# Kernel optimization log

Measured on AMD Instinct MI355X. Metric: run time of the kernel, lower is better.

## Reference

```python
import jax, jax.numpy as jnp
import numpy as np
import math

D_MODEL = 640
HEAD_DIM = 64
N_HEADS = 14
N_KV_HEADS = 2
HPK = N_HEADS // N_KV_HEADS  # 7
EPS = 1e-5
T = 2048
D_HALF = HEAD_DIM // 2


def setup_inputs() -> dict:
    key = jax.random.key(0)
    ks = jax.random.split(key, 10)
    x = jax.random.normal(ks[0], (1, D_MODEL, 1, T), dtype=jnp.float32)
    # rope tables: realistic cos/sin from standard rotary frequencies
    inv_freq = 1.0 / (10000.0 ** (jnp.arange(0, HEAD_DIM, 2, dtype=jnp.float32) / HEAD_DIM))
    ang = jnp.arange(T, dtype=jnp.float32)[:, None] * inv_freq[None, :]  # (T, 32)
    rope_cos = jnp.cos(ang)
    rope_sin = jnp.sin(ang)
    # causal additive mask (T, T)
    causal = jnp.tril(jnp.ones((T, T), dtype=bool))
    attn_mask = jnp.where(causal, 0.0, -1e9).astype(jnp.float32)
    norm_w = 1.0 + 0.02 * jax.random.normal(ks[1], (D_MODEL,), dtype=jnp.float32)
    qkv_dim = (N_HEADS + 2 * N_KV_HEADS) * HEAD_DIM  # 1152
    qkv_w = jax.random.normal(ks[2], (qkv_dim, D_MODEL), dtype=jnp.float32) * (D_MODEL ** -0.5)
    qkv_b = 0.02 * jax.random.normal(ks[3], (qkv_dim,), dtype=jnp.float32)
    o_w = jax.random.normal(ks[4], (D_MODEL, N_HEADS * HEAD_DIM), dtype=jnp.float32) * ((N_HEADS * HEAD_DIM) ** -0.5)
    o_b = 0.02 * jax.random.normal(ks[5], (D_MODEL,), dtype=jnp.float32)
    sinks = jax.random.normal(ks[6], (N_HEADS,), dtype=jnp.float32)
    return {"x": x, "rope_cos": rope_cos, "rope_sin": rope_sin, "attn_mask": attn_mask,
            "norm_w": norm_w, "qkv_w": qkv_w, "qkv_b": qkv_b, "o_w": o_w, "o_b": o_b,
            "sinks": sinks}


def _apply_rope(xf, n_heads, rope_cos, rope_sin):
    # xf: (1, T, n_heads*dh) -> interleaved rotary
    xr = xf.reshape(1, T, n_heads, HEAD_DIM)
    x1 = xr[..., 0::2]  # (1, T, n, d_half)
    x2 = xr[..., 1::2]
    cos = rope_cos[None, :, None, :]
    sin = rope_sin[None, :, None, :]
    o1 = x1 * cos - x2 * sin
    o2 = x2 * cos + x1 * sin
    return jnp.stack((o1, o2), axis=-1).reshape(1, T, n_heads * HEAD_DIM)


def reference(x, rope_cos, rope_sin, attn_mask, norm_w, qkv_w, qkv_b, o_w, o_b, sinks):
    nh, nkv, hpk, dh = N_HEADS, N_KV_HEADS, HPK, HEAD_DIM
    residual = x
    # RMSNorm over channel dim (axis=1)
    var = jnp.mean(x * x, axis=1, keepdims=True)
    normed = x * jax.lax.rsqrt(var + EPS) * norm_w.reshape(1, -1, 1, 1)
    # fused 1x1 conv QKV: (1, D, T) -> (1, T, qkv_dim)
    n2 = normed[:, :, 0, :]  # (1, D, T)
    qkv = jnp.einsum('bct,oc->bto', n2, qkv_w) + qkv_b
    q_dim = nh * dh
    kv_dim = nkv * dh
    q = qkv[:, :, :q_dim]
    k = qkv[:, :, q_dim:q_dim + kv_dim]
    v = qkv[:, :, q_dim + kv_dim:]
    q = _apply_rope(q, nh, rope_cos, rope_sin)
    k = _apply_rope(k, nkv, rope_cos, rope_sin)
    qk_scale = 1.0 / math.sqrt(math.sqrt(dh))
    q = q * qk_scale
    k = k * qk_scale
    q = q.reshape(1, T, nkv, hpk, dh)
    k = k.reshape(1, T, nkv, dh)
    v = v.reshape(1, T, nkv, dh)
    # GQA scores: (1, nkv, hpk, T, T)
    scores = jnp.einsum('btkgd,bskd->bkgts', q, k)
    scores = scores + attn_mask[None, None, None, :, :]
    # attention-sink logit column appended before softmax
    sink = (sinks * math.log(2.0)).reshape(1, nkv, hpk, 1, 1)
    sink_col = jnp.broadcast_to(sink, (1, nkv, hpk, T, 1))
    scores_with_sink = jnp.concatenate([scores, sink_col], axis=-1)
    attn_w = jax.nn.softmax(scores_with_sink, axis=-1)[..., :-1]
    # weighted values: (1, T, nkv, hpk, dh) -> (1, T, nh*dh)
    attn_out = jnp.einsum('bkgts,bskd->btkgd', attn_w, v).reshape(1, T, nh * dh)
    # output 1x1 conv + residual
    proj = jnp.einsum('bto,do->bdt', attn_out, o_w) + o_b.reshape(1, -1, 1)
    return residual + proj[:, :, None, :]
```

## Files before the change

### kernel.cpp

```cpp
#include <hip/hip_runtime.h>
#include <math.h>

#define T 2048
#define DM 640
#define NH 14
#define NKV 2
#define HPK 7
#define HD 64
#define QDIM 896
#define QKV_DIM 1152

constexpr float QK_SCALE2 = 0.35355339059327373f * 1.2011224087864498f;
constexpr float EPSF = 1e-5f;

typedef __attribute__((ext_vector_type(8))) short short8;
typedef __attribute__((ext_vector_type(4))) float float4v;
typedef unsigned short ush;

static __device__ __forceinline__ ush f2bf(float f) {
    union { float f; unsigned u; } v; v.f = f;
    unsigned r = v.u + 0x7fffu + ((v.u >> 16) & 1u);
    return (ush)(r >> 16);
}
static __device__ __forceinline__ float bf2f(ush s) {
    union { unsigned u; float f; } v; v.u = ((unsigned)s) << 16;
    return v.f;
}

__global__ __launch_bounds__(256) void rstd_kernel(
    const float* __restrict__ x, float* __restrict__ rstd)
{
    const int t0 = blockIdx.x * 64;
    const int tl = threadIdx.x & 63, cg = threadIdx.x >> 6;
    __shared__ float red[4][64];
    float ss = 0.f;
    for (int c = cg; c < DM; c += 4) {
        const float v = x[(size_t)c * T + t0 + tl];
        ss = fmaf(v, v, ss);
    }
    red[cg][tl] = ss;
    __syncthreads();
    if (threadIdx.x < 64) {
        const float s = red[0][tl] + red[1][tl] + red[2][tl] + red[3][tl];
        rstd[t0 + tl] = rsqrtf(s * (1.0f / DM) + EPSF);
    }
}

__global__ __launch_bounds__(256) void cast2_kernel(
    const float* __restrict__ a, ush* __restrict__ ah, ush* __restrict__ al, int na4,
    const float* __restrict__ b, ush* __restrict__ bh, ush* __restrict__ bl)
{
    const int i = blockIdx.x * 256 + threadIdx.x;
    const float* src; ush *dh, *dl; int j;
    if (i < na4) { src = a; dh = ah; dl = al; j = i; }
    else         { src = b; dh = bh; dl = bl; j = i - na4; }
    const float4 v = ((const float4*)src)[j];
    ushort4 h, l;
    h.x = f2bf(v.x); l.x = f2bf(v.x - bf2f(h.x));
    h.y = f2bf(v.y); l.y = f2bf(v.y - bf2f(h.y));
    h.z = f2bf(v.z); l.z = f2bf(v.z - bf2f(h.z));
    h.w = f2bf(v.w); l.w = f2bf(v.w - bf2f(h.w));
    ((ushort4*)dh)[j] = h;
    ((ushort4*)dl)[j] = l;
}

__global__ __launch_bounds__(256) void xnorm_kernel(
    const float* __restrict__ x, const float* __restrict__ norm_w,
    const float* __restrict__ rstd,
    ush* __restrict__ XnH, ush* __restrict__ XnL)
{
    const int tid = threadIdx.x;
    const int t0 = blockIdx.x * 64;
    const int c0 = blockIdx.y * 64;
    __shared__ float xs[64][65];

    #pragma unroll
    for (int it = 0; it < 4; ++it) {
        const int r = (tid >> 4) + it * 16;
        const int cl = (tid & 15) * 4;
        const float4 v = *(const float4*)&x[(size_t)(c0 + r) * T + t0 + cl];
        xs[r][cl + 0] = v.x; xs[r][cl + 1] = v.y;
        xs[r][cl + 2] = v.z; xs[r][cl + 3] = v.w;
    }
    __syncthreads();
    #pragma unroll
    for (int it = 0; it < 4; ++it) {
        const int tr = (tid >> 4) + it * 16;
        const int cl = (tid & 15) * 4;
        const float rs = rstd[t0 + tr];
        ushort4 h, l;
        const float v0 = xs[cl + 0][tr] * norm_w[c0 + cl + 0] * rs;
        const float v1 = xs[cl + 1][tr] * norm_w[c0 + cl + 1] * rs;
        const float v2 = xs[cl + 2][tr] * norm_w[c0 + cl + 2] * rs;
        const float v3 = xs[cl + 3][tr] * norm_w[c0 + cl + 3] * rs;
        h.x = f2bf(v0); l.x = f2bf(v0 - bf2f(h.x));
        h.y = f2bf(v1); l.y = f2bf(v1 - bf2f(h.y));
        h.z = f2bf(v2); l.z = f2bf(v2 - bf2f(h.z));
        h.w = f2bf(v3); l.w = f2bf(v3 - bf2f(h.w));
        *(ushort4*)&XnH[(size_t)(t0 + tr) * DM + c0 + cl] = h;
        *(ushort4*)&XnL[(size_t)(t0 + tr) * DM + c0 + cl] = l;
    }
}

#define QSX_H 0
#define QSX_L 8192
#define QSW_H 16384
#define QSW_L 24576

__global__ __launch_bounds__(256) void qkv_mfma_kernel(
    const ush* __restrict__ XnH, const ush* __restrict__ XnL,
    const ush* __restrict__ WH, const ush* __restrict__ WL,
    const float* __restrict__ qkv_b, const float* __restrict__ rope_cos,
    const float* __restrict__ rope_sin,
    ush* __restrict__ Qh, ush* __restrict__ Ql,
    ush* __restrict__ Kh, ush* __restrict__ Kl,
    ush* __restrict__ Vth, ush* __restrict__ Vtl)
{
    const int t0 = blockIdx.x * 64;
    const int o0 = blockIdx.y * 64;
    const int tid = threadIdx.x;
    const int wave = tid >> 6, lane = tid & 63;
    const int lg = lane >> 4, lq = lane & 15;
    const int wr = wave >> 1, wc = wave & 1;

    __shared__ __align__(16) unsigned char sm[65536];

    const int srow0 = tid >> 3, srow1 = srow0 + 32, scc = tid & 7;
    const int dst0 = srow0 * 128 + ((scc * 16) ^ ((srow0 & 7) << 4));
    const int dst1 = srow1 * 128 + ((scc * 16) ^ ((srow1 & 7) << 4));

    uint4 xh0, xl0, wh0, wl0, xh1, xl1, wh1, wl1;

#define QLOAD(c_) do { \
    xh0 = *(const uint4*)&XnH[(size_t)(t0 + srow0) * DM + (c_) + scc * 8]; \
    xl0 = *(const uint4*)&XnL[(size_t)(t0 + srow0) * DM + (c_) + scc * 8]; \
    wh0 = *(const uint4*)&WH [(size_t)(o0 + srow0) * DM + (c_) + scc * 8]; \
    wl0 = *(const uint4*)&WL [(size_t)(o0 + srow0) * DM + (c_) + scc * 8]; \
    xh1 = *(const uint4*)&XnH[(size_t)(t0 + srow1) * DM + (c_) + scc * 8]; \
    xl1 = *(const uint4*)&XnL[(size_t)(t0 + srow1) * DM + (c_) + scc * 8]; \
    wh1 = *(const uint4*)&WH [(size_t)(o0 + srow1) * DM + (c_) + scc * 8]; \
    wl1 = *(const uint4*)&WL [(size_t)(o0 + srow1) * DM + (c_) + scc * 8]; \
} while (0)

#define QSTORE(b_) do { \
    *(uint4*)((b_) + QSX_H + dst0) = xh0; \
    *(uint4*)((b_) + QSX_L + dst0) = xl0; \
    *(uint4*)((b_) + QSW_H + dst0) = wh0; \
    *(uint4*)((b_) + QSW_L + dst0) = wl0; \
    *(uint4*)((b_) + QSX_H + dst1) = xh1; \
    *(uint4*)((b_) + QSX_L + dst1) = xl1; \
    *(uint4*)((b_) + QSW_H + dst1) = wh1; \
    *(uint4*)((b_) + QSW_L + dst1) = wl1; \
} while (0)

    float4v acc[2][2];
    acc[0][0] = (float4v)0.f; acc[0][1] = (float4v)0.f;
    acc[1][0] = (float4v)0.f; acc[1][1] = (float4v)0.f;

    QLOAD(0);
    QSTORE(sm);
    int cur = 0;
    for (int s = 0; s < 10; ++s) {
        if (s < 9) QLOAD((s + 1) * 64);
        __syncthreads();
        const unsigned char* smb = sm + cur * 32768;
        #pragma unroll
        for (int kk = 0; kk < 2; ++kk) {
            short8 ah[2], al[2], bh[2], bl[2];
            #pragma unroll
            for (int nt = 0; nt < 2; ++nt) {
                const int row = wc * 32 + nt * 16 + lq;
                const int col = (kk * 64 + lg * 16) ^ ((row & 7) << 4);
                bh[nt] = *(const short8*)(smb + QSX_H + row * 128 + col);
                bl[nt] = *(const short8*)(smb + QSX_L + row * 128 + col);
            }
            #pragma unroll
            for (int mt = 0; mt < 2; ++mt) {
                const int row = wr * 32 + mt * 16 + lq;
                const int col = (kk * 64 + lg * 16) ^ ((row & 7) << 4);
                ah[mt] = *(const short8*)(smb + QSW_H + row * 128 + col);
                al[mt] = *(const short8*)(smb + QSW_L + row * 128 + col);
            }
            #pragma unroll
            for (int mt = 0; mt < 2; ++mt) {
                #pragma unroll
                for (int nt = 0; nt < 2; ++nt) {
                    acc[mt][nt] = __builtin_amdgcn_mfma_f32_16x16x32_bf16(ah[mt], bh[nt], acc[mt][nt], 0, 0, 0);
                    acc[mt][nt] = __builtin_amdgcn_mfma_f32_16x16x32_bf16(ah[mt], bl[nt], acc[mt][nt], 0, 0, 0);
                    acc[mt][nt] = __builtin_amdgcn_mfma_f32_16x16x32_bf16(al[mt], bh[nt], acc[mt][nt], 0, 0, 0);
                }
            }
        }
        if (s < 9) { QSTORE(sm + ((cur ^ 1) * 32768)); cur ^= 1; }
    }
#undef QLOAD
#undef QSTORE

    const int by = blockIdx.y;
    #pragma unroll
    for (int mt = 0; mt < 2; ++mt) {
        const int d0 = wr * 32 + mt * 16 + lg * 4;
        #pragma unroll
        for (int nt = 0; nt < 2; ++nt) {
            const int t = t0 + wc * 32 + nt * 16 + lq;
            if (by < 16) {
                const float e0 = acc[mt][nt][0] + qkv_b[o0 + d0 + 0];
                const float d1 = acc[mt][nt][1] + qkv_b[o0 + d0 + 1];
                const float e2 = acc[mt][nt][2] + qkv_b[o0 + d0 + 2];
                const float d3 = acc[mt][nt][3] + qkv_b[o0 + d0 + 3];
                const float c0v = rope_cos[t * 32 + (d0 >> 1)];
                const float s0v = rope_sin[t * 32 + (d0 >> 1)];
                const float c1v = rope_cos[t * 32 + (d0 >> 1) + 1];
                const float s1v = rope_sin[t * 32 + (d0 >> 1) + 1];
                const float r0 = (e0 * c0v - d1 * s0v) * QK_SCALE2;
                const float r1 = (d1 * c0v + e0 * s0v) * QK_SCALE2;
                const float r2 = (e2 * c1v - d3 * s1v) * QK_SCALE2;
                const float r3 = (d3 * c1v + e2 * s1v) * QK_SCALE2;
                ushort4 h, l;
                h.x = f2bf(r0); l.x = f2bf(r0 - bf2f(h.x));
                h.y = f2bf(r1); l.y = f2bf(r1 - bf2f(h.y));
                h.z = f2bf(r2); l.z = f2bf(r2 - bf2f(h.z));
                h.w = f2bf(r3); l.w = f2bf(r3 - bf2f(h.w));
                if (by < 14) {
                    *(ushort4*)&Qh[((size_t)(by * T + t)) * HD + d0] = h;
                    *(ushort4*)&Ql[((size_t)(by * T + t)) * HD + d0] = l;
                } else {
                    const int h2 = by - 14;
                    *(ushort4*)&Kh[((size_t)(h2 * T + t)) * HD + d0] = h;
                    *(ushort4*)&Kl[((size_t)(h2 * T + t)) * HD + d0] = l;
                }
            } else {
                const int h2 = by - 16;
                #pragma unroll
                for (int j = 0; j < 4; ++j) {
                    const float val = acc[mt][nt][j] + qkv_b[o0 + d0 + j];
                    const ush hh = f2bf(val);
                    Vth[((size_t)(h2 * HD + d0 + j)) * T + t] = hh;
                    Vtl[((size_t)(h2 * HD + d0 + j)) * T + t] = f2bf(val - bf2f(hh));
                }
            }
        }
    }
}

__global__ __launch_bounds__(256) void attn_mfma_kernel(
    const ush* __restrict__ Qh, const ush* __restrict__ Ql,
    const ush* __restrict__ Kh, const ush* __restrict__ Kl,
    const ush* __restrict__ Vth, const ush* __restrict__ Vtl,
    const float* __restrict__ sinks,
    ush* __restrict__ AOH, ush* __restrict__ AOL)
{
    const int qt = 31 - (int)blockIdx.x;
    const int h  = blockIdx.y;
    const int kvh = h / HPK;
    const int tid = threadIdx.x;
    const int wave = tid >> 6, lane = tid & 63;
    const int lg = lane >> 4, lq = lane & 15;
    const int qbase = qt * 64 + wave * 16;
    const int myq = qbase + lq;

    __shared__ __align__(16) unsigned char sm[2 * 32768 + 4 * 2304];
    unsigned int* Pl = (unsigned int*)(sm + 65536) + wave * (16 * 36);

    short8 qf[2][2];
    #pragma unroll
    for (int kk = 0; kk < 2; ++kk) {
        const size_t qoff = ((size_t)(h * T + myq)) * HD + kk * 32 + lg * 8;
        qf[kk][0] = *(const short8*)&Qh[qoff];
        qf[kk][1] = *(const short8*)&Ql[qoff];
    }

    float4v oacc[4];
    #pragma unroll
    for (int dt = 0; dt < 4; ++dt) oacc[dt] = (float4v)0.f;

    float m2 = sinks[h];
    float l  = 1.0f;

    const ush* Khp = Kh + (size_t)kvh * T * HD;
    const ush* Klp = Kl + (size_t)kvh * T * HD;
    const ush* Vhp = Vth + (size_t)kvh * HD * T;
    const ush* Vlp = Vtl + (size_t)kvh * HD * T;

    const int srow0 = tid >> 3, srow1 = srow0 + 32, scc = tid & 7;
    const int dst0 = srow0 * 128 + ((scc * 16) ^ ((srow0 & 7) << 4));
    const int dst1 = srow1 * 128 + ((scc * 16) ^ ((srow1 & 7) << 4));

    uint4 rk0h, rk0l, rv0h, rv0l, rk1h, rk1l, rv1h, rv1l;

#define ALOAD(kb_) do { \
    rk0h = *(const uint4*)(Khp + (size_t)((kb_) + srow0) * HD + scc * 8); \
    rk0l = *(const uint4*)(Klp + (size_t)((kb_) + srow0) * HD + scc * 8); \
    rv0h = *(const uint4*)(Vhp + (size_t)srow0 * T + (kb_) + scc * 8); \
    rv0l = *(const uint4*)(Vlp + (size_t)srow0 * T + (kb_) + scc * 8); \
    rk1h = *(const uint4*)(Khp + (size_t)((kb_) + srow1) * HD + scc * 8); \
    rk1l = *(const uint4*)(Klp + (size_t)((kb_) + srow1) * HD + scc * 8); \
    rv1h = *(const uint4*)(Vhp + (size_t)srow1 * T + (kb_) + scc * 8); \
    rv1l = *(const uint4*)(Vlp + (size_t)srow1 * T + (kb_) + scc * 8); \
} while (0)

#define ASTORE(b_) do { \
    *(uint4*)((b_) + 0     + dst0) = rk0h; \
    *(uint4*)((b_) + 8192  + dst0) = rk0l; \
    *(uint4*)((b_) + 16384 + dst0) = rv0h; \
    *(uint4*)((b_) + 24576 + dst0) = rv0l; \
    *(uint4*)((b_) + 0     + dst1) = rk1h; \
    *(uint4*)((b_) + 8192  + dst1) = rk1l; \
    *(uint4*)((b_) + 16384 + dst1) = rv1h; \
    *(uint4*)((b_) + 24576 + dst1) = rv1l; \
} while (0)

    ALOAD(0);
    ASTORE(sm);
    int cur = 0;

    for (int kt = 0; kt <= qt; ++kt) {
        const int kb = kt * 64;
        const bool more = (kt < qt);
        if (more) ALOAD(kb + 64);
        __syncthreads();
        unsigned char* smb = sm + cur * 32768;

        float4v st[4];
        #pragma unroll
        for (int t = 0; t < 4; ++t) st[t] = (float4v)0.f;
        #pragma unroll
        for (int t = 0; t < 4; ++t) {
            const int row = t * 16 + lq;
            const int rb = row * 128;
            const int sw = (row & 7) << 4;
            #pragma unroll
            for (int kk = 0; kk < 2; ++kk) {
                const int col = (kk * 64 + lg * 16) ^ sw;
                const short8 ah = *(const short8*)(smb + rb + col);
                const short8 al = *(const short8*)(smb + 8192 + rb + col);
                st[t] = __builtin_amdgcn_mfma_f32_16x16x32_bf16(ah, qf[kk][0], st[t], 0, 0, 0);
                st[t] = __builtin_amdgcn_mfma_f32_16x16x32_bf16(ah, qf[kk][1], st[t], 0, 0, 0);
                st[t] = __builtin_amdgcn_mfma_f32_16x16x32_bf16(al, qf[kk][0], st[t], 0, 0, 0);
            }
        }

        float pmax = -3e38f;
        #pragma unroll
        for (int t = 0; t < 4; ++t) {
            #pragma unroll
            for (int j = 0; j < 4; ++j) {
                const int key = kb + 16 * t + 4 * lg + j;
                const float s = (key > myq) ? -3e38f : st[t][j];
                st[t][j] = s;
                pmax = fmaxf(pmax, s);
            }
        }
        pmax = fmaxf(pmax, __shfl_xor(pmax, 16));
        pmax = fmaxf(pmax, __shfl_xor(pmax, 32));
        if (__any(pmax > m2)) {
            const float mnew = fmaxf(m2, pmax);
            const float corr = exp2f(m2 - mnew);
            l *= corr;
            #pragma unroll
            for (int dt = 0; dt < 4; ++dt) oacc[dt] *= corr;
            m2 = mnew;
        }
        float psum = 0.f;
        #pragma unroll
        for (int t = 0; t < 4; ++t) {
            #pragma unroll
            for (int j = 0; j < 4; ++j) {
                const float p = exp2f(st[t][j] - m2);
                st[t][j] = p;
                psum += p;
            }
        }
        psum += __shfl_xor(psum, 16);
        psum += __shfl_xor(psum, 32);
        l += psum;

        #pragma unroll
        for (int t = 0; t < 4; ++t) {
            #pragma unroll
            for (int j2 = 0; j2 < 2; ++j2) {
                const unsigned int u = (unsigned int)f2bf(st[t][2 * j2]) |
                                       ((unsigned int)f2bf(st[t][2 * j2 + 1]) << 16);
                Pl[lq * 36 + t * 8 + lg * 2 + j2] = u;
            }
        }

        #pragma unroll
        for (int c = 0; c < 2; ++c) {
            const short8 pf = *(const short8*)&Pl[lq * 36 + c * 16 + lg * 4];
            #pragma unroll
            for (int dt = 0; dt < 4; ++dt) {
                const int row = dt * 16 + lq;
                const int rb = row * 128;
                const int col = (c * 64 + lg * 16) ^ ((row & 7) << 4);
                const short8 vh = *(const short8*)(smb + 16384 + rb + col);
                const short8 vl = *(const short8*)(smb + 24576 + rb + col);
                oacc[dt] = __builtin_amdgcn_mfma_f32_16x16x32_bf16(vh, pf, oacc[dt], 0, 0, 0);
                oacc[dt] = __builtin_amdgcn_mfma_f32_16x16x32_bf16(vl, pf, oacc[dt], 0, 0, 0);
            }
        }

        if (more) { ASTORE(sm + ((cur ^ 1) * 32768)); cur ^= 1; }
    }
#undef ALOAD
#undef ASTORE

    const float invl = 1.0f / l;
    const int r = qbase + lq;
    const size_t obase = (size_t)r * QDIM + h * 64;
    #pragma unroll
    for (int dt = 0; dt < 4; ++dt) {
        ushort4 hh, ll;
        #pragma unroll
        for (int j = 0; j < 4; ++j) {
            const float val = oacc[dt][j] * invl;
            const ush hv = f2bf(val);
            ((ush*)&hh)[j] = hv;
            ((ush*)&ll)[j] = f2bf(val - bf2f(hv));
        }
        *(ushort4*)&AOH[obase + dt * 16 + lg * 4] = hh;
        *(ushort4*)&AOL[obase + dt * 16 + lg * 4] = ll;
    }
}

#define PSA_H 0
#define PSA_L 8192
#define PSW_H 16384
#define PSW_L 24576

__global__ __launch_bounds__(256) void oproj_mfma_kernel(
    const ush* __restrict__ AOH, const ush* __restrict__ AOL,
    const ush* __restrict__ OWH, const ush* __restrict__ OWL,
    const float* __restrict__ o_b, const float* __restrict__ x,
    float* __restrict__ out)
{
    const int t0 = blockIdx.x * 64;
    const int c0 = blockIdx.y * 64;
    const int tid = threadIdx.x;
    const int wave = tid >> 6, lane = tid & 63;
    const int lg = lane >> 4, lq = lane & 15;
    const int wr = wave >> 1, wc = wave & 1;

    __shared__ __align__(16) unsigned char sm[65536];

    const int srow0 = tid >> 3, srow1 = srow0 + 32, scc = tid & 7;
    const int dst0 = srow0 * 128 + ((scc * 16) ^ ((srow0 & 7) << 4));
    const int dst1 = srow1 * 128 + ((scc * 16) ^ ((srow1 & 7) << 4));

    uint4 xh0, xl0, wh0, wl0, xh1, xl1, wh1, wl1;

#define PLOAD(k_) do { \
    xh0 = *(const uint4*)&AOH[(size_t)(t0 + srow0) * QDIM + (k_) + scc * 8]; \
    xl0 = *(const uint4*)&AOL[(size_t)(t0 + srow0) * QDIM + (k_) + scc * 8]; \
    wh0 = *(const uint4*)&OWH[(size_t)(c0 + srow0) * QDIM + (k_) + scc * 8]; \
    wl0 = *(const uint4*)&OWL[(size_t)(c0 + srow0) * QDIM + (k_) + scc * 8]; \
    xh1 = *(const uint4*)&AOH[(size_t)(t0 + srow1) * QDIM + (k_) + scc * 8]; \
    xl1 = *(const uint4*)&AOL[(size_t)(t0 + srow1) * QDIM + (k_) + scc * 8]; \
    wh1 = *(const uint4*)&OWH[(size_t)(c0 + srow1) * QDIM + (k_) + scc * 8]; \
    wl1 = *(const uint4*)&OWL[(size_t)(c0 + srow1) * QDIM + (k_) + scc * 8]; \
} while (0)

#define PSTORE(b_) do { \
    *(uint4*)((b_) + PSA_H + dst0) = xh0; \
    *(uint4*)((b_) + PSA_L + dst0) = xl0; \
    *(uint4*)((b_) + PSW_H + dst0) = wh0; \
    *(uint4*)((b_) + PSW_L + dst0) = wl0; \
    *(uint4*)((b_) + PSA_H + dst1) = xh1; \
    *(uint4*)((b_) + PSA_L + dst1) = xl1; \
    *(uint4*)((b_) + PSW_H + dst1) = wh1; \
    *(uint4*)((b_) + PSW_L + dst1) = wl1; \
} while (0)

    float4v acc[2][2];
    acc[0][0] = (float4v)0.f; acc[0][1] = (float4v)0.f;
    acc[1][0] = (float4v)0.f; acc[1][1] = (float4v)0.f;

    PLOAD(0);
    PSTORE(sm);
    int cur = 0;
    for (int s = 0; s < 14; ++s) {
        if (s < 13) PLOAD((s + 1) * 64);
        __syncthreads();
        const unsigned char* smb = sm + cur * 32768;
        #pragma unroll
        for (int kk = 0; kk < 2; ++kk) {
            short8 ah[2], al[2], bh[2], bl[2];
            #pragma unroll
            for (int nt = 0; nt < 2; ++nt) {
                const int row = wc * 32 + nt * 16 + lq;
                const int col = (kk * 64 + lg * 16) ^ ((row & 7) << 4);
                bh[nt] = *(const short8*)(smb + PSA_H + row * 128 + col);
                bl[nt] = *(const short8*)(smb + PSA_L + row * 128 + col);
            }
            #pragma unroll
            for (int mt = 0; mt < 2; ++mt) {
                const int row = wr * 32 + mt * 16 + lq;
                const int col = (kk * 64 + lg * 16) ^ ((row & 7) << 4);
                ah[mt] = *(const short8*)(smb + PSW_H + row * 128 + col);
                al[mt] = *(const short8*)(smb + PSW_L + row * 128 + col);
            }
            #pragma unroll
            for (int mt = 0; mt < 2; ++mt) {
                #pragma unroll
                for (int nt = 0; nt < 2; ++nt) {
                    acc[mt][nt] = __builtin_amdgcn_mfma_f32_16x16x32_bf16(ah[mt], bh[nt], acc[mt][nt], 0, 0, 0);
                    acc[mt][nt] = __builtin_amdgcn_mfma_f32_16x16x32_bf16(ah[mt], bl[nt], acc[mt][nt], 0, 0, 0);
                    acc[mt][nt] = __builtin_amdgcn_mfma_f32_16x16x32_bf16(al[mt], bh[nt], acc[mt][nt], 0, 0, 0);
                }
            }
        }
        if (s < 13) { PSTORE(sm + ((cur ^ 1) * 32768)); cur ^= 1; }
    }
#undef PLOAD
#undef PSTORE

    #pragma unroll
    for (int mt = 0; mt < 2; ++mt) {
        const int cb = c0 + wr * 32 + mt * 16 + lg * 4;
        #pragma unroll
        for (int nt = 0; nt < 2; ++nt) {
            const int t = t0 + wc * 32 + nt * 16 + lq;
            #pragma unroll
            for (int j = 0; j < 4; ++j) {
                const int c = cb + j;
                out[(size_t)c * T + t] = acc[mt][nt][j] + o_b[c] + x[(size_t)c * T + t];
            }
        }
    }
}

extern "C" void kernel_launch(void* const* d_in, const int* in_sizes, int n_in,
                              void* d_out, int out_size, void* d_ws, size_t ws_size,
                              hipStream_t stream) {
    const float* x        = (const float*)d_in[0];
    const float* rope_cos = (const float*)d_in[1];
    const float* rope_sin = (const float*)d_in[2];
    const float* norm_w   = (const float*)d_in[4];
    const float* qkv_w    = (const float*)d_in[5];
    const float* qkv_b    = (const float*)d_in[6];
    const float* o_w      = (const float*)d_in[7];
    const float* o_b      = (const float*)d_in[8];
    const float* sinks    = (const float*)d_in[9];
    float* out = (float*)d_out;

    float* ws   = (float*)d_ws;
    float* rstd = ws;
    ush* bws = (ush*)(rstd + 2048);
    ush* Qh  = bws;
    ush* Ql  = Qh  + 1835008;
    ush* Kh  = Ql  + 1835008;
    ush* Kl  = Kh  + 262144;
    ush* Vth = Kl  + 262144;
    ush* Vtl = Vth + 262144;
    ush* XnH = Vtl + 262144;
    ush* XnL = XnH + 1310720;
    ush* WqH = XnL + 1310720;
    ush* WqL = WqH + 737280;
    ush* OWH = WqL + 737280;
    ush* OWL = OWH + 573440;
    ush* AOH = OWL + 573440;
    ush* AOL = AOH + 1835008;

    rstd_kernel<<<32, 256, 0, stream>>>(x, rstd);
    cast2_kernel<<<1280, 256, 0, stream>>>(qkv_w, WqH, WqL, QKV_DIM * DM / 4,
                                           o_w, OWH, OWL);
    xnorm_kernel<<<dim3(32, 10), 256, 0, stream>>>(x, norm_w, rstd, XnH, XnL);
    qkv_mfma_kernel<<<dim3(32, 18), 256, 0, stream>>>(
        XnH, XnL, WqH, WqL, qkv_b, rope_cos, rope_sin, Qh, Ql, Kh, Kl, Vth, Vtl);
    attn_mfma_kernel<<<dim3(32, NH), 256, 0, stream>>>(
        Qh, Ql, Kh, Kl, Vth, Vtl, sinks, AOH, AOL);
    oproj_mfma_kernel<<<dim3(32, 10), 256, 0, stream>>>(AOH, AOL, OWH, OWL, o_b, x, out);
}
```

Measured before the change: 250.8 us.

## Split attention KV range across two blocks and merge with combine kernel

```diff
diff --git a/kernel.cpp b/kernel.cpp
--- a/kernel.cpp
+++ b/kernel.cpp
@@ -161,8 +161,8 @@
     QSTORE(sm);
     int cur = 0;
     for (int s = 0; s < 10; ++s) {
+        __syncthreads();
         if (s < 9) QLOAD((s + 1) * 64);
-        __syncthreads();
         const unsigned char* smb = sm + cur * 32768;
         #pragma unroll
         for (int kk = 0; kk < 2; ++kk) {
@@ -248,10 +248,11 @@
     const ush* __restrict__ Kh, const ush* __restrict__ Kl,
     const ush* __restrict__ Vth, const ush* __restrict__ Vtl,
     const float* __restrict__ sinks,
-    ush* __restrict__ AOH, ush* __restrict__ AOL)
+    float* __restrict__ Opart, float* __restrict__ Mpart, float* __restrict__ Lpart)
 {
     const int qt = 31 - (int)blockIdx.x;
     const int h  = blockIdx.y;
+    const int kc = blockIdx.z;
     const int kvh = h / HPK;
     const int tid = threadIdx.x;
     const int wave = tid >> 6, lane = tid & 63;
@@ -274,8 +275,9 @@
     #pragma unroll
     for (int dt = 0; dt < 4; ++dt) oacc[dt] = (float4v)0.f;
 
-    float m2 = sinks[h];
-    float l  = 1.0f;
+    float m2, l;
+    if (kc == 0) { m2 = sinks[h]; l = 1.0f; }
+    else         { m2 = -3e38f;   l = 0.0f; }
 
     const ush* Khp = Kh + (size_t)kvh * T * HD;
     const ush* Klp = Kl + (size_t)kvh * T * HD;
@@ -310,15 +312,15 @@
     *(uint4*)((b_) + 24576 + dst1) = rv1l; \
 } while (0)
 
-    ALOAD(0);
-    ASTORE(sm);
+    const int nt_cnt = (qt >= kc) ? ((qt - kc) >> 1) + 1 : 0;
+    if (nt_cnt > 0) { ALOAD(kc * 64); ASTORE(sm); }
     int cur = 0;
 
-    for (int kt = 0; kt <= qt; ++kt) {
+    for (int i = 0; i < nt_cnt; ++i) {
+        const int kt = kc + 2 * i;
         const int kb = kt * 64;
-        const bool more = (kt < qt);
-        if (more) ALOAD(kb + 64);
         __syncthreads();
+        if (i + 1 < nt_cnt) ALOAD(kb + 128);
         unsigned char* smb = sm + cur * 32768;
 
         float4v st[4];
@@ -400,26 +402,58 @@
             }
         }
 
-        if (more) { ASTORE(sm + ((cur ^ 1) * 32768)); cur ^= 1; }
+        if (i + 1 < nt_cnt) { ASTORE(sm + ((cur ^ 1) * 32768)); cur ^= 1; }
     }
 #undef ALOAD
 #undef ASTORE
 
-    const float invl = 1.0f / l;
     const int r = qbase + lq;
-    const size_t obase = (size_t)r * QDIM + h * 64;
+    const int pb = (h * 2 + kc) * 64;
     #pragma unroll
     for (int dt = 0; dt < 4; ++dt) {
+        #pragma unroll
+        for (int j = 0; j < 4; ++j) {
+            const int d = dt * 16 + lg * 4 + j;
+            Opart[(size_t)(pb + d) * T + r] = oacc[dt][j];
+        }
+    }
+    if (lane < 16) {
+        Mpart[(size_t)(h * 2 + kc) * T + r] = m2;
+        Lpart[(size_t)(h * 2 + kc) * T + r] = l;
+    }
+}
+
+__global__ __launch_bounds__(256) void attn_combine_kernel(
+    const float* __restrict__ Opart, const float* __restrict__ Mpart,
+    const float* __restrict__ Lpart,
+    ush* __restrict__ AOH, ush* __restrict__ AOL)
+{
+    const int idx = blockIdx.x * 256 + threadIdx.x;
+    const int h = idx >> 11;
+    const int r = idx & (T - 1);
+
+    const float m0 = Mpart[(h * 2 + 0) * T + r], l0 = Lpart[(h * 2 + 0) * T + r];
+    const float m1 = Mpart[(h * 2 + 1) * T + r], l1 = Lpart[(h * 2 + 1) * T + r];
+    const float M = fmaxf(m0, m1);
+    float w0 = exp2f(m0 - M), w1 = exp2f(m1 - M);
+    const float L = l0 * w0 + l1 * w1;
+    const float invL = 1.0f / L;
+    w0 *= invL; w1 *= invL;
+
+    #pragma unroll
+    for (int d4 = 0; d4 < 16; ++d4) {
         ushort4 hh, ll;
         #pragma unroll
         for (int j = 0; j < 4; ++j) {
-            const float val = oacc[dt][j] * invl;
-            const ush hv = f2bf(val);
+            const int d = d4 * 4 + j;
+            const float acc = Opart[((h * 2 + 0) * 64 + d) * (size_t)T + r] * w0
+                            + Opart[((h * 2 + 1) * 64 + d) * (size_t)T + r] * w1;
+            const ush hv = f2bf(acc);
             ((ush*)&hh)[j] = hv;
-            ((ush*)&ll)[j] = f2bf(val - bf2f(hv));
-        }
-        *(ushort4*)&AOH[obase + dt * 16 + lg * 4] = hh;
-        *(ushort4*)&AOL[obase + dt * 16 + lg * 4] = ll;
+            ((ush*)&ll)[j] = f2bf(acc - bf2f(hv));
+        }
+        *(ushort4*)&AOH[(size_t)r * QDIM + h * 64 + d4 * 4] = hh;
+        *(ushort4*)&AOL[(size_t)r * QDIM + h * 64 + d4 * 4] = ll;
     }
 }
 
@@ -479,8 +513,8 @@
     PSTORE(sm);
     int cur = 0;
     for (int s = 0; s < 14; ++s) {
+        __syncthreads();
         if (s < 13) PLOAD((s + 1) * 64);
-        __syncthreads();
         const unsigned char* smb = sm + cur * 32768;
         #pragma unroll
         for (int kk = 0; kk < 2; ++kk) {
@@ -543,9 +577,12 @@
     const float* sinks    = (const float*)d_in[9];
     float* out = (float*)d_out;
 
-    float* ws   = (float*)d_ws;
-    float* rstd = ws;
-    ush* bws = (ush*)(rstd + 2048);
+    float* ws    = (float*)d_ws;
+    float* rstd  = ws;
+    float* Opart = rstd + 2048;
+    float* Mpart = Opart + 3670016;
+    float* Lpart = Mpart + 57344;
+    ush* bws = (ush*)(Lpart + 57344);
     ush* Qh  = bws;
     ush* Ql  = Qh  + 1835008;
     ush* Kh  = Ql  + 1835008;
@@ -567,7 +604,8 @@
     xnorm_kernel<<<dim3(32, 10), 256, 0, stream>>>(x, norm_w, rstd, XnH, XnL);
     qkv_mfma_kernel<<<dim3(32, 18), 256, 0, stream>>>(
         XnH, XnL, WqH, WqL, qkv_b, rope_cos, rope_sin, Qh, Ql, Kh, Kl, Vth, Vtl);
-    attn_mfma_kernel<<<dim3(32, NH), 256, 0, stream>>>(
-        Qh, Ql, Kh, Kl, Vth, Vtl, sinks, AOH, AOL);
+    attn_mfma_kernel<<<dim3(32, NH, 2), 256, 0, stream>>>(
+        Qh, Ql, Kh, Kl, Vth, Vtl, sinks, Opart, Mpart, Lpart);
+    attn_combine_kernel<<<NH * T / 256, 256, 0, stream>>>(Opart, Mpart, Lpart, AOH, AOL);
     oproj_mfma_kernel<<<dim3(32, 10), 256, 0, stream>>>(AOH, AOL, OWH, OWL, o_b, x, out);
 }
```

Result: slower. 261.6 us (+4.3%).
